# Kernel optimization log

Hardware: AMD Instinct MI355X
Metric: run time of the kernel (lower is better)

Reference implementation:

```python
import jax, jax.numpy as jnp
import numpy as np

POOL_SIZE = 7
NUM_ROIS = 600
H, W, C = 96, 96, 1024


def setup_inputs() -> dict:
    key = jax.random.key(0)
    k_img, k_xy, k_wh = jax.random.split(key, 3)
    img = jax.random.normal(k_img, (1, H, W, C), dtype=jnp.float32)
    # (x, y) top-left corners and (w, h) sizes, all integer feature-map coords
    xy = jax.random.randint(k_xy, (1, NUM_ROIS, 2), 0, 64, dtype=jnp.int32)
    wh = jax.random.randint(k_wh, (1, NUM_ROIS, 2), 4, 36, dtype=jnp.int32)
    rois = jnp.concatenate([xy, wh], axis=-1)  # (1, num_rois, 4) as (x, y, w, h)
    return {"img": img, "rois": rois}


def _pool_one_roi(img2d, roi):
    """img2d: (H, W, C) float; roi: (4,) int32 (x, y, w, h).
    Reproduces tf.image.resize_images (bilinear, align_corners=False, TF1
    semantics: src = dst * in/out) applied to the crop img[y:y+h, x:x+w],
    without materializing the dynamic-shape crop."""
    x, y, w, h = roi[0], roi[1], roi[2], roi[3]
    w = jnp.maximum(w, 1)
    h = jnp.maximum(h, 1)
    out_idx = jnp.arange(POOL_SIZE, dtype=jnp.float32)
    # source coords within the crop
    in_y = out_idx * (h.astype(jnp.float32) / POOL_SIZE)
    in_x = out_idx * (w.astype(jnp.float32) / POOL_SIZE)
    y0 = jnp.floor(in_y).astype(jnp.int32)
    x0 = jnp.floor(in_x).astype(jnp.int32)
    y1 = jnp.minimum(y0 + 1, h - 1)
    x1 = jnp.minimum(x0 + 1, w - 1)
    fy = (in_y - y0.astype(jnp.float32))[:, None, None]  # (P,1,1)
    fx = (in_x - x0.astype(jnp.float32))[None, :, None]  # (1,P,1)
    # map crop-local indices into the full image, clamp for safety
    r0 = jnp.clip(y + y0, 0, H - 1)
    r1 = jnp.clip(y + y1, 0, H - 1)
    c0 = jnp.clip(x + x0, 0, W - 1)
    c1 = jnp.clip(x + x1, 0, W - 1)
    top = img2d[r0[:, None], c0[None, :]] * (1.0 - fx) + img2d[r0[:, None], c1[None, :]] * fx
    bot = img2d[r1[:, None], c0[None, :]] * (1.0 - fx) + img2d[r1[:, None], c1[None, :]] * fx
    return top * (1.0 - fy) + bot * fy  # (P, P, C)


def reference(img, rois):
    img2d = img[0]          # (H, W, C)
    rois2d = rois[0]        # (num_rois, 4)
    out = jax.vmap(_pool_one_roi, in_axes=(None, 0))(img2d, rois2d)
    return out[None]        # (1, num_rois, P, P, C)
```

## Files before the change

### kernel.cpp

```cpp
#include <hip/hip_runtime.h>

#define POOL 7
#define NUM_ROIS 600
#define IMG_H 96
#define IMG_W 96
#define IMG_C 1024

__global__ __launch_bounds__(256) void roi_pool_kernel(
    const float* __restrict__ img,
    const int* __restrict__ rois,
    float* __restrict__ out)
{
    const int b   = blockIdx.x;
    const int roi = b / (POOL * POOL);
    const int p   = b - roi * (POOL * POOL);
    const int py  = p / POOL;
    const int px  = p - py * POOL;

    const int4 r = *(const int4*)(rois + roi * 4);
    const int x = r.x;
    const int y = r.y;
    const int w = max(r.z, 1);
    const int h = max(r.w, 1);

    const float in_y = (float)py * ((float)h / (float)POOL);
    const float in_x = (float)px * ((float)w / (float)POOL);
    const int y0 = (int)floorf(in_y);
    const int x0 = (int)floorf(in_x);
    const int y1 = min(y0 + 1, h - 1);
    const int x1 = min(x0 + 1, w - 1);
    const float fy = in_y - (float)y0;
    const float fx = in_x - (float)x0;
    const float gy = 1.0f - fy;
    const float gx = 1.0f - fx;

    const int R0 = min(max(y + y0, 0), IMG_H - 1);
    const int R1 = min(max(y + y1, 0), IMG_H - 1);
    const int C0 = min(max(x + x0, 0), IMG_W - 1);
    const int C1 = min(max(x + x1, 0), IMG_W - 1);

    const int ch = threadIdx.x * 4;
    const float4 v00 = *(const float4*)(img + (size_t)(R0 * IMG_W + C0) * IMG_C + ch);
    const float4 v01 = *(const float4*)(img + (size_t)(R0 * IMG_W + C1) * IMG_C + ch);
    const float4 v10 = *(const float4*)(img + (size_t)(R1 * IMG_W + C0) * IMG_C + ch);
    const float4 v11 = *(const float4*)(img + (size_t)(R1 * IMG_W + C1) * IMG_C + ch);

    float4 o;
    o.x = (v00.x * gx + v01.x * fx) * gy + (v10.x * gx + v11.x * fx) * fy;
    o.y = (v00.y * gx + v01.y * fx) * gy + (v10.y * gx + v11.y * fx) * fy;
    o.z = (v00.z * gx + v01.z * fx) * gy + (v10.z * gx + v11.z * fx) * fy;
    o.w = (v00.w * gx + v01.w * fx) * gy + (v10.w * gx + v11.w * fx) * fy;

    *(float4*)(out + (size_t)b * IMG_C + ch) = o;
}

extern "C" void kernel_launch(void* const* d_in, const int* in_sizes, int n_in,
                              void* d_out, int out_size, void* d_ws, size_t ws_size,
                              hipStream_t stream) {
    const float* img  = (const float*)d_in[0];
    const int*   rois = (const int*)d_in[1];
    float*       out  = (float*)d_out;

    const int nblocks = NUM_ROIS * POOL * POOL;
    roi_pool_kernel<<<nblocks, 256, 0, stream>>>(img, rois, out);
}
```

Baseline: 187.1 us.

## Process a full pooled row per block with XCD-aware ROI mapping and nontemporal stores

Each block now computes all seven pooled columns of one output row, cutting the grid by a factor of seven and hoisting per-row setup out of the column loop. Block indices are remapped so that all rows of a ROI are scheduled on the same XCD, improving L2 reuse of shared image rows. Output writes use nontemporal stores to avoid polluting cache with the large streaming output. Fewer blocks reduce parallelism per wave and increase per-thread register use.

```diff
diff --git a/kernel.cpp b/kernel.cpp
--- a/kernel.cpp
+++ b/kernel.cpp
@@ -6,16 +6,19 @@
 #define IMG_W 96
 #define IMG_C 1024
 
+typedef float v4f __attribute__((ext_vector_type(4)));
+
 __global__ __launch_bounds__(256) void roi_pool_kernel(
     const float* __restrict__ img,
     const int* __restrict__ rois,
     float* __restrict__ out)
 {
     const int b   = blockIdx.x;
-    const int roi = b / (POOL * POOL);
-    const int p   = b - roi * (POOL * POOL);
-    const int py  = p / POOL;
-    const int px  = p - py * POOL;
+    const int xcd = b & 7;
+    const int j   = b >> 3;
+    const int py  = j % POOL;
+    const int k   = j / POOL;
+    const int roi = k * 8 + xcd;
 
     const int4 r = *(const int4*)(rois + roi * 4);
     const int x = r.x;
@@ -23,35 +26,41 @@
     const int w = max(r.z, 1);
     const int h = max(r.w, 1);
 
-    const float in_y = (float)py * ((float)h / (float)POOL);
-    const float in_x = (float)px * ((float)w / (float)POOL);
+    const float sy = (float)h / (float)POOL;
+    const float sx = (float)w / (float)POOL;
+
+    const float in_y = (float)py * sy;
     const int y0 = (int)floorf(in_y);
-    const int x0 = (int)floorf(in_x);
     const int y1 = min(y0 + 1, h - 1);
-    const int x1 = min(x0 + 1, w - 1);
     const float fy = in_y - (float)y0;
-    const float fx = in_x - (float)x0;
     const float gy = 1.0f - fy;
-    const float gx = 1.0f - fx;
-
     const int R0 = min(max(y + y0, 0), IMG_H - 1);
     const int R1 = min(max(y + y1, 0), IMG_H - 1);
-    const int C0 = min(max(x + x0, 0), IMG_W - 1);
-    const int C1 = min(max(x + x1, 0), IMG_W - 1);
 
     const int ch = threadIdx.x * 4;
-    const float4 v00 = *(const float4*)(img + (size_t)(R0 * IMG_W + C0) * IMG_C + ch);
-    const float4 v01 = *(const float4*)(img + (size_t)(R0 * IMG_W + C1) * IMG_C + ch);
-    const float4 v10 = *(const float4*)(img + (size_t)(R1 * IMG_W + C0) * IMG_C + ch);
-    const float4 v11 = *(const float4*)(img + (size_t)(R1 * IMG_W + C1) * IMG_C + ch);
+    const float* row0 = img + (size_t)R0 * IMG_W * IMG_C + ch;
+    const float* row1 = img + (size_t)R1 * IMG_W * IMG_C + ch;
+    float* outp = out + ((size_t)roi * POOL * POOL + (size_t)py * POOL) * IMG_C + ch;
 
-    float4 o;
-    o.x = (v00.x * gx + v01.x * fx) * gy + (v10.x * gx + v11.x * fx) * fy;
-    o.y = (v00.y * gx + v01.y * fx) * gy + (v10.y * gx + v11.y * fx) * fy;
-    o.z = (v00.z * gx + v01.z * fx) * gy + (v10.z * gx + v11.z * fx) * fy;
-    o.w = (v00.w * gx + v01.w * fx) * gy + (v10.w * gx + v11.w * fx) * fy;
+#pragma unroll
+    for (int px = 0; px < POOL; ++px) {
+        const float in_x = (float)px * sx;
+        const int x0 = (int)floorf(in_x);
+        const int x1 = min(x0 + 1, w - 1);
+        const float fx = in_x - (float)x0;
+        const float gx = 1.0f - fx;
+        const int C0 = min(max(x + x0, 0), IMG_W - 1);
+        const int C1 = min(max(x + x1, 0), IMG_W - 1);
 
-    *(float4*)(out + (size_t)b * IMG_C + ch) = o;
+        const v4f v00 = *(const v4f*)(row0 + (size_t)C0 * IMG_C);
+        const v4f v01 = *(const v4f*)(row0 + (size_t)C1 * IMG_C);
+        const v4f v10 = *(const v4f*)(row1 + (size_t)C0 * IMG_C);
+        const v4f v11 = *(const v4f*)(row1 + (size_t)C1 * IMG_C);
+
+        const v4f o = (v00 * gx + v01 * fx) * gy + (v10 * gx + v11 * fx) * fy;
+
+        __builtin_nontemporal_store(o, (v4f*)(outp + (size_t)px * IMG_C));
+    }
 }
 
 extern "C" void kernel_launch(void* const* d_in, const int* in_sizes, int n_in,
@@ -61,6 +70,6 @@
     const int*   rois = (const int*)d_in[1];
     float*       out  = (float*)d_out;
 
-    const int nblocks = NUM_ROIS * POOL * POOL;
+    const int nblocks = NUM_ROIS * POOL;
     roi_pool_kernel<<<nblocks, 256, 0, stream>>>(img, rois, out);
 }
```

Measured after the change: 181.8 us. -2.8%, faster.
